# Optimization experiments

Hardware: AMD Instinct MI355X
Metric: run time of the kernel (lower is better)

## Reference

```python
import jax, jax.numpy as jnp
import numpy as np

B, L = 64, 200
NQ = 1024          # n_question == output_dim
NPID = 4096
D = 256            # q_embed_dim
H = 512            # hidden_dim
Q = 1024           # output_dim
L2 = 1e-05


def setup_inputs() -> dict:
    key = jax.random.key(0)
    ks = jax.random.split(key, 20)
    q_data = jax.random.randint(ks[0], (B, L), 1, NQ + 1)          # question ids in [1, NQ]
    ans = jax.random.randint(ks[1], (B, L), 0, 2)
    qa_data = q_data + NQ * ans                                     # encoded (q, answer)
    pid_data = jax.random.randint(ks[2], (B, L), 0, NPID + 1)
    matrix = jax.random.uniform(ks[3], (Q, Q), jnp.float32) * 0.05  # p_c_relations
    u = jax.random.uniform(ks[4], (B, L))
    target = jnp.where(u < 0.1, -1.0, jnp.where(u < 0.55, 0.0, 1.0)).astype(jnp.float32)
    s = 0.05
    q_emb = jax.random.normal(ks[5], (NQ + 1, D), jnp.float32) * s
    qa_emb = jax.random.normal(ks[6], (2, D), jnp.float32) * s
    q_emb_diff = jax.random.normal(ks[7], (NQ + 1, D), jnp.float32) * s
    qa_emb_diff = jax.random.normal(ks[8], (2 * NQ + 1, D), jnp.float32) * s
    diff_parm = jax.random.normal(ks[9], (NPID + 1, 1), jnp.float32) * s
    gs = 1.0 / np.sqrt(H).astype(np.float32)
    w_ih = jax.random.uniform(ks[10], (3 * H, 2 * D), jnp.float32, -gs, gs)
    w_hh = jax.random.uniform(ks[11], (3 * H, H), jnp.float32, -gs, gs)
    b_ih = jax.random.uniform(ks[12], (3 * H,), jnp.float32, -gs, gs)
    b_hh = jax.random.uniform(ks[13], (3 * H,), jnp.float32, -gs, gs)
    fc_w = jax.random.normal(ks[14], (Q, H), jnp.float32) * 0.02
    fc_b = jnp.zeros((Q,), jnp.float32)
    return dict(q_data=q_data, qa_data=qa_data, pid_data=pid_data, matrix=matrix,
                target=target, q_emb=q_emb, qa_emb=qa_emb, q_emb_diff=q_emb_diff,
                qa_emb_diff=qa_emb_diff, diff_parm=diff_parm, w_ih=w_ih, w_hh=w_hh,
                b_ih=b_ih, b_hh=b_hh, fc_w=fc_w, fc_b=fc_b)


def _gru(x, w_ih, w_hh, b_ih, b_hh):
    # PyTorch GRU, single layer, batch_first. x: [B, L, In]
    xg = jnp.einsum('bli,gi->blg', x, w_ih) + b_ih          # [B, L, 3H]
    def step(h, xg_t):
        hg = h @ w_hh.T + b_hh
        xr, xz, xn = jnp.split(xg_t, 3, axis=-1)
        hr, hz, hn = jnp.split(hg, 3, axis=-1)
        r = jax.nn.sigmoid(xr + hr)
        z = jax.nn.sigmoid(xz + hz)
        n = jnp.tanh(xn + r * hn)
        h_new = (1.0 - z) * n + z * h
        return h_new, h_new
    h0 = jnp.zeros((x.shape[0], w_hh.shape[1]), x.dtype)
    _, hs = jax.lax.scan(step, h0, xg.transpose(1, 0, 2))
    return hs.transpose(1, 0, 2)                             # [B, L, H]


def reference(q_data, qa_data, pid_data, matrix, target, q_emb, qa_emb,
              q_emb_diff, qa_emb_diff, diff_parm, w_ih, w_hh, b_ih, b_hh,
              fc_w, fc_b):
    q_embed = q_emb[q_data]                                  # [B, L, D]
    qa = (qa_data - q_data) // NQ                            # answer in {0,1}
    qa_embed = qa_emb[qa] + q_embed
    pid_embed = diff_parm[pid_data]                          # [B, L, 1]
    q_embed2 = q_embed + pid_embed * q_emb_diff[q_data]
    qa_embed2 = qa_embed + pid_embed * qa_emb_diff[qa]
    c_reg = (pid_embed ** 2).sum() * L2

    x = jnp.concatenate([qa_embed2, q_embed2], axis=-1)      # [B, L, 2D]
    gru_out = _gru(x, w_ih, w_hh, b_ih, b_hh)
    gru_out = jnp.einsum('blh,qh->blq', gru_out, fc_w) + fc_b  # [B, L, Q]

    got = jnp.einsum('blq,kq->blk', gru_out, matrix)         # [B, L, Q]
    master = jnp.where(got >= 0.4, 1.0, got)                 # threshold-to-1 only
    # mastery of the question asked at step t: master[b, t, q-1]
    mvals = jnp.take_along_axis(master, (q_data - 1)[..., None], axis=2)[..., 0]  # [B, L]

    f32 = jnp.float32
    eq = (q_data[:, :, None] == q_data[:, None, :]).astype(f32)   # [B, t, k]
    t_idx = jnp.arange(L)
    tri_strict = (t_idx[:, None] > t_idx[None, :]).astype(f32)    # k < t
    tri_incl = (t_idx[:, None] >= t_idx[None, :]).astype(f32)     # k <= t
    mast = (mvals == 1.0).astype(f32)
    notm = (mvals == 0.0).astype(f32)
    qa1 = (qa == 1).astype(f32)
    qa0 = 1.0 - qa1
    base = eq * tri_strict                                        # [B, L, L]
    mc = jnp.einsum('btk,bk->bt', base, qa1 * mast)   # master_correct
    mi = jnp.einsum('btk,bk->bt', base, qa0 * mast)   # master_incorrect
    nmc = jnp.einsum('btk,bk->bt', base, qa0 * notm)  # no_master_correct
    aa = jnp.einsum('btk,tk->bt', eq, tri_incl)       # answered_all (>= 1)

    arB = jnp.arange(B)
    idx = q_data - 1

    def dina_step(carry, xs):
        guess, slip = carry                            # [B, Q] each
        i_t, m_t, qa_t, mc_t, mi_t, nmc_t, aa_t = xs   # [B] each
        g_upd = jnp.where(m_t == 1.0, mc_t / aa_t,
                          jnp.where(qa_t == 0, 1.0 - nmc_t / aa_t, nmc_t / aa_t))
        upd_slip = (m_t == 1.0) & (qa_t == 0)
        new_g = jnp.where(upd_slip, guess[arB, i_t], g_upd)
        new_s = jnp.where(upd_slip, mi_t / aa_t, slip[arB, i_t])
        guess = guess.at[arB, i_t].set(new_g)
        slip = slip.at[arB, i_t].set(new_s)
        p = (1.0 - new_s) * (m_t * new_g + (1.0 - new_s) * (1.0 - m_t))
        return (guess, slip), p

    init = (jnp.zeros((B, Q), f32), jnp.zeros((B, Q), f32))
    xs = (idx.T, mvals.T, qa.T, mc.T, mi.T, nmc.T, aa.T)
    _, ps = jax.lax.scan(dina_step, init, xs)          # [L, B]
    preds = ps.T.reshape(-1)                           # [B*L]

    labels = target.reshape(-1)
    mask = labels > -0.9
    preds_d = jax.lax.stop_gradient(preds)             # torch detaches via torch.tensor()
    mse_sum = (((preds_d - labels) ** 2) * mask.astype(f32)).sum()
    loss = mse_sum + c_reg
    return (loss, jax.nn.sigmoid(preds_d), mask.sum())
```

## Files before the change

### kernel.cpp

```cpp
#include <hip/hip_runtime.h>
#include <hip/hip_bf16.h>
#include <math.h>

#define BB 64
#define LL 200
#define NQ 1024
#define DD 256
#define HH 512
#define QQ 1024
#define G3 1536
#define BL 12800
#define GBLK 256

#define OFF_ACC   ((size_t)0)
#define OFF_CELLS ((size_t)16)
#define OFF_HA    ((size_t)1056)
#define OFF_AQ    (OFF_HA + 65536)
#define OFF_DQ    (OFF_AQ + 1574400)
#define OFF_BQA   (OFF_DQ + 1574400)
#define OFF_CQA   (OFF_BQA + 3072)
#define OFF_WSUM  (OFF_CQA + 3072)
#define OFF_FCWT  (OFF_WSUM + 393216)
#define OFF_M2    (OFF_FCWT + 524288)
#define OFF_MB    (OFF_M2 + 524288)
#define OFF_XG    (OFF_MB + 1024)
#define OFF_GRUT  (OFF_XG + 19660800)
#define OFF_QINT  (OFF_GRUT + 6553600)
#define OFF_QAINT (OFF_QINT + 12800)
#define OFF_PIDF  (OFF_QAINT + 12800)
#define OFF_MVAL  (OFF_PIDF + 12800)
#define OFF_MC    (OFF_MVAL + 12800)
#define OFF_MI    (OFF_MC + 12800)
#define OFF_NMC   (OFF_MI + 12800)
#define OFF_AA    (OFF_NMC + 12800)
#define OFF_PREDS (OFF_AA + 12800)

typedef float f32x4 __attribute__((ext_vector_type(4)));

__device__ __forceinline__ float wave_sum64(float v) {
    #pragma unroll
    for (int o = 32; o > 0; o >>= 1) v += __shfl_down(v, o, 64);
    return v;
}

__device__ __forceinline__ f32x4 llc_load4(const float* p) {
    f32x4 v;
    asm volatile("global_load_dwordx4 %0, %1, off sc0 sc1" : "=v"(v) : "v"(p));
    return v;
}
__device__ __forceinline__ void llc_wait2(f32x4& a, f32x4& b) {
    asm volatile("s_waitcnt vmcnt(0)" : "+v"(a), "+v"(b));
}
__device__ __forceinline__ void llc_store1(float* p, float v) {
    asm volatile("global_store_dword %0, %1, off sc0 sc1" :: "v"(p), "v"(v) : "memory");
}

__device__ __forceinline__ float quad_sum(float v) {
    float t1 = __int_as_float(__builtin_amdgcn_update_dpp(
        0, __float_as_int(v), 0xB1, 0xF, 0xF, true));
    v += t1;
    float t2 = __int_as_float(__builtin_amdgcn_update_dpp(
        0, __float_as_int(v), 0x4E, 0xF, 0xF, true));
    return v + t2;
}

__global__ __launch_bounds__(256) void prep_meta(
    const int* __restrict__ q_data, const int* __restrict__ qa_data,
    const int* __restrict__ pid_data, const float* __restrict__ diff_parm,
    int* __restrict__ qint, int* __restrict__ qaint, float* __restrict__ pidf,
    float* __restrict__ acc)
{
    int r = blockIdx.x * 256 + threadIdx.x;
    float pp = 0.f;
    if (r < BL) {
        int q = q_data[r];
        qint[r] = q;
        qaint[r] = (qa_data[r] - q) / NQ;
        float pid = diff_parm[pid_data[r]];
        pidf[r] = pid;
        pp = pid * pid;
    }
    pp = wave_sum64(pp);
    __shared__ float sm[4];
    int lane = threadIdx.x & 63, w = threadIdx.x >> 6;
    if (lane == 0) sm[w] = pp;
    __syncthreads();
    if (threadIdx.x == 0) atomicAdd(&acc[0], sm[0] + sm[1] + sm[2] + sm[3]);
}

__global__ __launch_bounds__(256) void wsum_kernel(const float* __restrict__ w_ih,
                                                   float* __restrict__ wsum)
{
    int g = blockIdx.x, d = threadIdx.x;
    wsum[(size_t)g * DD + d] = w_ih[(size_t)g * 2 * DD + d] + w_ih[(size_t)g * 2 * DD + DD + d];
}

__global__ __launch_bounds__(256) void transpose_kernel(const float* __restrict__ in,
                                                        float* __restrict__ out, int R, int C)
{
    __shared__ float tile[32][33];
    int r0 = blockIdx.y * 32, c0 = blockIdx.x * 32;
    int tx = threadIdx.x & 31, ty = threadIdx.x >> 5;
    #pragma unroll
    for (int i = 0; i < 32; i += 8) {
        int r = r0 + ty + i, c = c0 + tx;
        if (r < R && c < C) tile[ty + i][tx] = in[(size_t)r * C + c];
    }
    __syncthreads();
    #pragma unroll
    for (int i = 0; i < 32; i += 8) {
        int c = c0 + ty + i, r = r0 + tx;
        if (c < C && r < R) out[(size_t)c * R + r] = tile[tx][ty + i];
    }
}

__global__ __launch_bounds__(256) void gemm_nt_dual(
    const float* __restrict__ A0, const float* __restrict__ A1, int lda,
    const float* __restrict__ B0, const float* __restrict__ B1, int ldb0, int ldb1,
    float* __restrict__ C0, float* __restrict__ C1, int ldc,
    int M, int N, int K,
    const float* __restrict__ bias0, const float* __restrict__ bias1)
{
    const int z = blockIdx.z;
    const float* A = z ? A1 : A0;
    const float* B = z ? B1 : B0;
    float* C = z ? C1 : C0;
    const int ldb = z ? ldb1 : ldb0;
    const float* bias = z ? bias1 : bias0;

    __shared__ float As[16][65];
    __shared__ float Bs[16][65];
    const int bm = blockIdx.y * 64, bn = blockIdx.x * 64;
    const int tid = threadIdx.x;
    const int tx = tid & 15, ty = tid >> 4;
    const int mm = tid >> 4, kk = tid & 15;
    float acc[4][4] = {};
    float ar[4], br[4];
    #pragma unroll
    for (int i = 0; i < 4; ++i) {
        int m = bm + mm + 16 * i;
        ar[i] = (m < M) ? A[(size_t)m * lda + kk] : 0.f;
        int n = bn + mm + 16 * i;
        br[i] = (n < N) ? B[(size_t)n * ldb + kk] : 0.f;
    }
    for (int k0 = 0; k0 < K; k0 += 16) {
        #pragma unroll
        for (int i = 0; i < 4; ++i) { As[kk][mm + 16 * i] = ar[i]; Bs[kk][mm + 16 * i] = br[i]; }
        __syncthreads();
        int kn = k0 + 16;
        if (kn < K) {
            #pragma unroll
            for (int i = 0; i < 4; ++i) {
                int m = bm + mm + 16 * i;
                ar[i] = (m < M) ? A[(size_t)m * lda + kn + kk] : 0.f;
                int n = bn + mm + 16 * i;
                br[i] = (n < N) ? B[(size_t)n * ldb + kn + kk] : 0.f;
            }
        }
        #pragma unroll
        for (int kq = 0; kq < 16; ++kq) {
            float a[4], b[4];
            #pragma unroll
            for (int i = 0; i < 4; ++i) a[i] = As[kq][ty * 4 + i];
            #pragma unroll
            for (int j = 0; j < 4; ++j) b[j] = Bs[kq][tx * 4 + j];
            #pragma unroll
            for (int i = 0; i < 4; ++i)
                #pragma unroll
                for (int j = 0; j < 4; ++j) acc[i][j] += a[i] * b[j];
        }
        __syncthreads();
    }
    #pragma unroll
    for (int i = 0; i < 4; ++i) {
        int m = bm + ty * 4 + i;
        if (m >= M) continue;
        #pragma unroll
        for (int j = 0; j < 4; ++j) {
            int n = bn + tx * 4 + j;
            if (n >= N) continue;
            C[(size_t)m * ldc + n] = acc[i][j] + (bias ? bias[n] : 0.f);
        }
    }
}

__global__ __launch_bounds__(256) void gemm_nt_splitk(
    const float* __restrict__ Ain, int lda,
    const float* __restrict__ Bin, int ldb,
    float* __restrict__ Cp, int ldc,
    int M, int N, int K4)
{
    const int z = blockIdx.z;
    const float* A = Ain + (size_t)z * K4;
    const float* B = Bin + (size_t)z * K4;
    float* C = Cp + (size_t)z * M * ldc;

    __shared__ float As[16][65];
    __shared__ float Bs[16][65];
    const int bm = blockIdx.y * 64, bn = blockIdx.x * 64;
    const int tid = threadIdx.x;
    const int tx = tid & 15, ty = tid >> 4;
    const int mm = tid >> 4, kk = tid & 15;
    float acc[4][4] = {};
    float ar[4], br[4];
    #pragma unroll
    for (int i = 0; i < 4; ++i) {
        int m = bm + mm + 16 * i;
        ar[i] = (m < M) ? A[(size_t)m * lda + kk] : 0.f;
        int n = bn + mm + 16 * i;
        br[i] = (n < N) ? B[(size_t)n * ldb + kk] : 0.f;
    }
    for (int k0 = 0; k0 < K4; k0 += 16) {
        #pragma unroll
        for (int i = 0; i < 4; ++i) { As[kk][mm + 16 * i] = ar[i]; Bs[kk][mm + 16 * i] = br[i]; }
        __syncthreads();
        int kn = k0 + 16;
        if (kn < K4) {
            #pragma unroll
            for (int i = 0; i < 4; ++i) {
                int m = bm + mm + 16 * i;
                ar[i] = (m < M) ? A[(size_t)m * lda + kn + kk] : 0.f;
                int n = bn + mm + 16 * i;
                br[i] = (n < N) ? B[(size_t)n * ldb + kn + kk] : 0.f;
            }
        }
        #pragma unroll
        for (int kq = 0; kq < 16; ++kq) {
            float a[4], b[4];
            #pragma unroll
            for (int i = 0; i < 4; ++i) a[i] = As[kq][ty * 4 + i];
            #pragma unroll
            for (int j = 0; j < 4; ++j) b[j] = Bs[kq][tx * 4 + j];
            #pragma unroll
            for (int i = 0; i < 4; ++i)
                #pragma unroll
                for (int j = 0; j < 4; ++j) acc[i][j] += a[i] * b[j];
        }
        __syncthreads();
    }
    #pragma unroll
    for (int i = 0; i < 4; ++i) {
        int m = bm + ty * 4 + i;
        if (m >= M) continue;
        #pragma unroll
        for (int j = 0; j < 4; ++j) {
            int n = bn + tx * 4 + j;
            if (n >= N) continue;
            C[(size_t)m * ldc + n] = acc[i][j];
        }
    }
}

__global__ __launch_bounds__(256) void reduce4_kernel(const float* __restrict__ p,
                                                      float* __restrict__ o, int n)
{
    int i = blockIdx.x * 256 + threadIdx.x;
    if (i < n) o[i] = p[i] + p[n + i] + p[2 * n + i] + p[3 * n + i];
}

__global__ __launch_bounds__(256) void mb_kernel(const float* __restrict__ matrix,
                                                 const float* __restrict__ fc_b,
                                                 float* __restrict__ mb)
{
    int k = blockIdx.x;
    float s = 0.f;
    for (int q = threadIdx.x; q < QQ; q += 256) s += matrix[(size_t)k * QQ + q] * fc_b[q];
    s = wave_sum64(s);
    __shared__ float sm[4];
    int lane = threadIdx.x & 63, w = threadIdx.x >> 6;
    if (lane == 0) sm[w] = s;
    __syncthreads();
    if (threadIdx.x == 0) mb[k] = sm[0] + sm[1] + sm[2] + sm[3];
}

__global__ __launch_bounds__(512) void xgt_kernel(
    const float* __restrict__ Aq, const float* __restrict__ Bqa,
    const float* __restrict__ Cqa, const float* __restrict__ Dq,
    const int* __restrict__ qint, const int* __restrict__ qaint,
    const float* __restrict__ pidf, float* __restrict__ xgT)
{
    const int t = blockIdx.x;
    __shared__ float tile[64][129];
    __shared__ int qs[BB];
    __shared__ int qas[BB];
    __shared__ float ps[BB];
    const int tid = threadIdx.x;
    if (tid < BB) {
        qs[tid] = qint[tid * LL + t];
        qas[tid] = qaint[tid * LL + t];
        ps[tid] = pidf[tid * LL + t];
    }
    __syncthreads();
    for (int g0 = 0; g0 < G3; g0 += 128) {
        #pragma unroll
        for (int it = 0; it < 16; ++it) {
            int idx = it * 512 + tid;
            int b = idx >> 7, gg = idx & 127;
            int g = g0 + gg;
            int q = qs[b], qa = qas[b];
            float pid = ps[b];
            tile[b][gg] = Aq[(size_t)q * G3 + g] + Bqa[(size_t)qa * G3 + g]
                        + pid * (Cqa[(size_t)qa * G3 + g] + Dq[(size_t)q * G3 + g]);
        }
        __syncthreads();
        #pragma unroll
        for (int it = 0; it < 16; ++it) {
            int idx = it * 512 + tid;
            int gg = idx >> 6, b = idx & 63;
            xgT[((size_t)t * G3 + g0 + gg) * BB + b] = tile[b][gg];
        }
        __syncthreads();
    }
}

__global__ __launch_bounds__(512) void gru_persist(
    const float* __restrict__ xgT,
    const float* __restrict__ w_hh,
    const float* __restrict__ b_hh,
    float* __restrict__ hA,
    float* __restrict__ gruT2,
    unsigned int* __restrict__ cells)
{
    __shared__ float hs[8][512];
    __shared__ float part[8][3][16][8];

    const int tid = threadIdx.x;
    const int bid = blockIdx.x;
    const int bg = bid >> 5;
    const int j0 = (bid & 31) * 16;
    const int wv = tid >> 6;
    const int lane = tid & 63;
    const int g = lane >> 2;
    const int s = lane & 3;

    f32x4 ws4[3][4];
    #pragma unroll
    for (int gate = 0; gate < 3; ++gate) {
        #pragma unroll
        for (int q = 0; q < 4; ++q) {
            ws4[gate][q] = *(const f32x4*)&w_hh[(size_t)(gate * HH + j0 + g) * HH
                                                + wv * 64 + q * 16 + s * 4];
        }
    }

    const int eu = tid >> 3;
    const int eb = tid & 7;
    float bhr = 0.f, bhz = 0.f, bhn = 0.f;
    if (tid < 128) {
        bhr = b_hh[j0 + eu];
        bhz = b_hh[HH + j0 + eu];
        bhn = b_hh[2 * HH + j0 + eu];
    }

    const int b0 = lane >> 4;
    const int c0 = (lane & 15) * 4;

    int cur = 0;
    for (int t = 0; t < LL; ++t) {
        float xr = 0.f, xz = 0.f, xn = 0.f;
        if (tid < 128) {
            const float* xb = xgT + (size_t)t * G3 * BB;
            int col = bg * 8 + eb;
            xr = xb[(size_t)(j0 + eu) * BB + col];
            xz = xb[(size_t)(HH + j0 + eu) * BB + col];
            xn = xb[(size_t)(2 * HH + j0 + eu) * BB + col];
        }
        if (t && tid < 64) {
            const unsigned want = (unsigned)t;
            for (;;) {
                unsigned v = want;
                if (lane < 32)
                    v = __hip_atomic_load(&cells[(bg * 32 + lane) * 4],
                                          __ATOMIC_RELAXED, __HIP_MEMORY_SCOPE_AGENT);
                if (__all((int)(v >= want))) break;
                __builtin_amdgcn_s_sleep(2);
            }
        }
        __syncthreads();

        const float* hcur = hA + (size_t)cur * (HH * BB);
        {
            const float* p0 = hcur + (size_t)(bg * 8 + b0) * HH + wv * 64 + c0;
            f32x4 va = llc_load4(p0);
            f32x4 vb = llc_load4(p0 + 4 * HH);
            llc_wait2(va, vb);
            *(f32x4*)&hs[wv][b0 * 64 + ((c0 + 8 * b0) & 63)] = va;
            *(f32x4*)&hs[wv][(b0 + 4) * 64 + ((c0 + 8 * b0 + 32) & 63)] = vb;
        }

        float acc[3][8];
        #pragma unroll
        for (int gate = 0; gate < 3; ++gate) {
            #pragma unroll
            for (int b = 0; b < 8; ++b) acc[gate][b] = 0.f;
        }
        #pragma unroll
        for (int q = 0; q < 4; ++q) {
            const int cb = q * 16 + s * 4;
            #pragma unroll
            for (int b = 0; b < 8; ++b) {
                f32x4 h4 = *(const f32x4*)&hs[wv][b * 64 + ((cb + 8 * b) & 63)];
                #pragma unroll
                for (int gate = 0; gate < 3; ++gate) {
                    acc[gate][b] += ws4[gate][q].x * h4.x + ws4[gate][q].y * h4.y
                                  + ws4[gate][q].z * h4.z + ws4[gate][q].w * h4.w;
                }
            }
        }

        #pragma unroll
        for (int gate = 0; gate < 3; ++gate) {
            #pragma unroll
            for (int b = 0; b < 8; ++b) acc[gate][b] = quad_sum(acc[gate][b]);
        }

        if (s < 3) {
            const int rot = (2 * ((g >> 2) + s)) & 7;
            #pragma unroll
            for (int hp = 0; hp < 4; ++hp) {
                const int b = hp * 2;
                float e0 = (s == 0) ? acc[0][b]     : (s == 1) ? acc[1][b]     : acc[2][b];
                float e1 = (s == 0) ? acc[0][b + 1] : (s == 1) ? acc[1][b + 1] : acc[2][b + 1];
                const int bp = (b + rot) & 7;
                *(float2*)&part[wv][s][g][bp] = make_float2(e0, e1);
            }
        }
        __syncthreads();

        if (tid < 128) {
            const int rb = eu >> 2;
            const int bp0 = (eb + 2 * (rb + 0)) & 7;
            const int bp1 = (eb + 2 * (rb + 1)) & 7;
            const int bp2 = (eb + 2 * (rb + 2)) & 7;
            float sg0 = 0.f, sg1 = 0.f, sg2 = 0.f;
            #pragma unroll
            for (int w = 0; w < 8; ++w) {
                sg0 += part[w][0][eu][bp0];
                sg1 += part[w][1][eu][bp1];
                sg2 += part[w][2][eu][bp2];
            }
            const int ku = j0 + eu;
            float hprev = hs[ku >> 6][eb * 64 + (((ku & 63) + 8 * eb) & 63)];
            float r = 1.f / (1.f + expf(-(xr + sg0 + bhr)));
            float z = 1.f / (1.f + expf(-(xz + sg1 + bhz)));
            float n = tanhf(xn + r * (sg2 + bhn));
            float hn = (1.f - z) * n + z * hprev;
            llc_store1(hA + (size_t)(cur ^ 1) * (HH * BB) + (size_t)(bg * 8 + eb) * HH + ku, hn);
            gruT2[((size_t)t * BB + bg * 8 + eb) * HH + ku] = hn;
            asm volatile("s_waitcnt vmcnt(0)" ::: "memory");
        }
        __syncthreads();
        if (tid == 0 && t + 1 < LL)
            __hip_atomic_fetch_add(&cells[bid * 4], 1u,
                                   __ATOMIC_RELAXED, __HIP_MEMORY_SCOPE_AGENT);
        cur ^= 1;
    }
}

__global__ __launch_bounds__(256) void mval_kernel(
    const float* __restrict__ gruT2,
    const float* __restrict__ M2,
    const float* __restrict__ mb,
    const int* __restrict__ qint,
    float* __restrict__ mval)
{
    int t = blockIdx.x;
    int wave = threadIdx.x >> 6, l = threadIdx.x & 63;
    for (int ii = 0; ii < 16; ++ii) {
        int b = wave * 16 + ii;
        int q = qint[b * LL + t] - 1;
        const float4* hp = (const float4*)(gruT2 + ((size_t)t * BB + b) * HH);
        const float4* mp = (const float4*)(M2 + (size_t)q * HH);
        float4 h0 = hp[l], m0 = mp[l];
        float4 h1 = hp[64 + l], m1 = mp[64 + l];
        float acc = h0.x * m0.x + h0.y * m0.y + h0.z * m0.z + h0.w * m0.w
                  + h1.x * m1.x + h1.y * m1.y + h1.z * m1.z + h1.w * m1.w;
        acc = wave_sum64(acc);
        if (l == 0) {
            float sv = acc + mb[q];
            mval[b * LL + t] = (sv >= 0.4f) ? 1.0f : sv;
        }
    }
}

__global__ __launch_bounds__(256) void stats_kernel(
    const int* __restrict__ qint, const int* __restrict__ qaint,
    const float* __restrict__ mval,
    float* __restrict__ mc, float* __restrict__ mi,
    float* __restrict__ nmc, float* __restrict__ aa)
{
    int b = blockIdx.x, tid = threadIdx.x;
    __shared__ int qs[LL];
    __shared__ int qas[LL];
    __shared__ float mv[LL];
    if (tid < LL) {
        qs[tid] = qint[b * LL + tid];
        qas[tid] = qaint[b * LL + tid];
        mv[tid] = mval[b * LL + tid];
    }
    __syncthreads();
    int t = tid;
    if (t < LL) {
        int qt = qs[t];
        float smc = 0.f, smi = 0.f, snmc = 0.f, saa = 0.f;
        for (int k = 0; k <= t; ++k) {
            if (qs[k] == qt) {
                saa += 1.f;
                if (k < t) {
                    float mk = (mv[k] == 1.f) ? 1.f : 0.f;
                    float nk = (mv[k] == 0.f) ? 1.f : 0.f;
                    float a1 = (qas[k] == 1) ? 1.f : 0.f;
                    smc += a1 * mk;
                    smi += (1.f - a1) * mk;
                    snmc += (1.f - a1) * nk;
                }
            }
        }
        mc[b * LL + t] = smc;
        mi[b * LL + t] = smi;
        nmc[b * LL + t] = snmc;
        aa[b * LL + t] = saa;
    }
}

__global__ __launch_bounds__(256) void dina_kernel(
    const int* __restrict__ qint, const int* __restrict__ qaint,
    const float* __restrict__ mval,
    const float* __restrict__ mc, const float* __restrict__ mi,
    const float* __restrict__ nmc, const float* __restrict__ aa,
    float* __restrict__ preds)
{
    int b = blockIdx.x, tid = threadIdx.x;
    __shared__ float guess[QQ], slip[QQ];
    __shared__ float s_m[LL], s_mc[LL], s_mi[LL], s_nmc[LL], s_aa[LL];
    __shared__ int s_i[LL], s_qa[LL];
    for (int i = tid; i < QQ; i += 256) { guess[i] = 0.f; slip[i] = 0.f; }
    if (tid < LL) {
        s_m[tid] = mval[b * LL + tid];
        s_mc[tid] = mc[b * LL + tid];
        s_mi[tid] = mi[b * LL + tid];
        s_nmc[tid] = nmc[b * LL + tid];
        s_aa[tid] = aa[b * LL + tid];
        s_i[tid] = qint[b * LL + tid] - 1;
        s_qa[tid] = qaint[b * LL + tid];
    }
    __syncthreads();
    if (tid == 0) {
        for (int t = 0; t < LL; ++t) {
            int i = s_i[t];
            float m = s_m[t];
            int qa = s_qa[t];
            float aat = s_aa[t];
            float g_upd = (m == 1.f) ? s_mc[t] / aat
                          : ((qa == 0) ? 1.f - s_nmc[t] / aat : s_nmc[t] / aat);
            bool us = (m == 1.f) && (qa == 0);
            float ng = us ? guess[i] : g_upd;
            float ns = us ? s_mi[t] / aat : slip[i];
            guess[i] = ng;
            slip[i] = ns;
            preds[b * LL + t] = (1.f - ns) * (m * ng + (1.f - ns) * (1.f - m));
        }
    }
}

__global__ __launch_bounds__(256) void loss_kernel(
    const float* __restrict__ preds, const float* __restrict__ target,
    float* __restrict__ out, float* __restrict__ acc)
{
    int r = blockIdx.x * 256 + threadIdx.x;
    float lm = 0.f, lc = 0.f;
    if (r < BL) {
        float p = preds[r], lab = target[r];
        float msk = (lab > -0.9f) ? 1.f : 0.f;
        float d = p - lab;
        lm = d * d * msk;
        lc = msk;
        out[1 + r] = 1.f / (1.f + expf(-p));
    }
    lm = wave_sum64(lm);
    lc = wave_sum64(lc);
    __shared__ float sm[4], sc[4];
    int lane = threadIdx.x & 63, w = threadIdx.x >> 6;
    if (lane == 0) { sm[w] = lm; sc[w] = lc; }
    __syncthreads();
    if (threadIdx.x == 0) {
        atomicAdd(&acc[1], sm[0] + sm[1] + sm[2] + sm[3]);
        atomicAdd(&acc[2], sc[0] + sc[1] + sc[2] + sc[3]);
    }
}

__global__ void final_kernel(const float* __restrict__ acc, float* __restrict__ out)
{
    out[0] = acc[1] + acc[0] * 1e-5f;
    out[1 + BL] = acc[2];
}

extern "C" void kernel_launch(void* const* d_in, const int* in_sizes, int n_in,
                              void* d_out, int out_size, void* d_ws, size_t ws_size,
                              hipStream_t stream) {
    const int* q_data = (const int*)d_in[0];
    const int* qa_data = (const int*)d_in[1];
    const int* pid_data = (const int*)d_in[2];
    const float* matrix = (const float*)d_in[3];
    const float* target = (const float*)d_in[4];
    const float* q_emb = (const float*)d_in[5];
    const float* qa_emb = (const float*)d_in[6];
    const float* q_emb_diff = (const float*)d_in[7];
    const float* qa_emb_diff = (const float*)d_in[8];
    const float* diff_parm = (const float*)d_in[9];
    const float* w_ih = (const float*)d_in[10];
    const float* w_hh = (const float*)d_in[11];
    const float* b_ih = (const float*)d_in[12];
    const float* b_hh = (const float*)d_in[13];
    const float* fc_w = (const float*)d_in[14];
    const float* fc_b = (const float*)d_in[15];
    float* out = (float*)d_out;
    float* W = (float*)d_ws;

    float* acc = W + OFF_ACC;
    unsigned int* cells = (unsigned int*)(W + OFF_CELLS);
    float* hA = W + OFF_HA;
    float* Aq = W + OFF_AQ;
    float* Dq = W + OFF_DQ;
    float* Bqa = W + OFF_BQA;
    float* Cqa = W + OFF_CQA;
    float* wsum = W + OFF_WSUM;
    float* fcwT = W + OFF_FCWT;
    float* M2 = W + OFF_M2;
    float* mb = W + OFF_MB;
    float* xgT = W + OFF_XG;
    float* m2parts = W + OFF_XG;
    float* gruT2 = W + OFF_GRUT;
    int* qint = (int*)(W + OFF_QINT);
    int* qaint = (int*)(W + OFF_QAINT);
    float* pidf = W + OFF_PIDF;
    float* mval = W + OFF_MVAL;
    float* mc = W + OFF_MC;
    float* mi = W + OFF_MI;
    float* nmc = W + OFF_NMC;
    float* aa = W + OFF_AA;
    float* preds = W + OFF_PREDS;

    hipMemsetAsync(W, 0, (OFF_HA + 2 * HH * BB) * sizeof(float), stream);

    prep_meta<<<50, 256, 0, stream>>>(q_data, qa_data, pid_data, diff_parm,
                                      qint, qaint, pidf, acc);
    wsum_kernel<<<G3, 256, 0, stream>>>(w_ih, wsum);
    transpose_kernel<<<dim3(16, 32), 256, 0, stream>>>(fc_w, fcwT, QQ, HH);

    gemm_nt_dual<<<dim3(24, 1, 2), 256, 0, stream>>>(
        qa_emb, qa_emb_diff, DD, w_ih, w_ih, 2 * DD, 2 * DD,
        Bqa, Cqa, G3, 2, G3, DD, b_ih, nullptr);
    gemm_nt_dual<<<dim3(24, 17, 2), 256, 0, stream>>>(
        q_emb, q_emb_diff, DD, wsum, w_ih + DD, DD, 2 * DD,
        Aq, Dq, G3, NQ + 1, G3, DD, nullptr, nullptr);
    gemm_nt_splitk<<<dim3(8, 16, 4), 256, 0, stream>>>(
        matrix, QQ, fcwT, QQ, m2parts, HH, QQ, HH, QQ / 4);
    reduce4_kernel<<<2048, 256, 0, stream>>>(m2parts, M2, QQ * HH);
    mb_kernel<<<QQ, 256, 0, stream>>>(matrix, fc_b, mb);

    xgt_kernel<<<LL, 512, 0, stream>>>(Aq, Bqa, Cqa, Dq, qint, qaint, pidf, xgT);

    gru_persist<<<GBLK, 512, 0, stream>>>(xgT, w_hh, b_hh, hA, gruT2, cells);

    mval_kernel<<<LL, 256, 0, stream>>>(gruT2, M2, mb, qint, mval);
    stats_kernel<<<BB, 256, 0, stream>>>(qint, qaint, mval, mc, mi, nmc, aa);
    dina_kernel<<<BB, 256, 0, stream>>>(qint, qaint, mval, mc, mi, nmc, aa, preds);
    loss_kernel<<<50, 256, 0, stream>>>(preds, target, out, acc);
    final_kernel<<<1, 1, 0, stream>>>(acc, out);
}
```

Baseline: 1.160 ms.

## Compute M2 and mb in extra blocks of the persistent GRU kernel

Removes the separate transpose, split-K GEMM, reduce and mb kernels. Their work (matrix·fc_wᵀ and matrix·fc_b) now runs in 130 extra worker blocks appended to the persistent GRU launch, so it overlaps with the latency-bound recurrence. GRU blocks raise their wave priority with s_setprio. The step counter now uses an atomic store of t+1 instead of an atomic add. The risk is that worker blocks take CU resources or memory bandwidth from GRU blocks. If the 386 blocks are not all resident at once, the spin-wait sync could also be affected.

```diff
diff --git a/kernel.cpp b/kernel.cpp
--- a/kernel.cpp
+++ b/kernel.cpp
@@ -11,6 +11,7 @@
 #define G3 1536
 #define BL 12800
 #define GBLK 256
+#define NWRK 130
 
 #define OFF_ACC   ((size_t)0)
 #define OFF_CELLS ((size_t)16)
@@ -95,25 +96,6 @@
     wsum[(size_t)g * DD + d] = w_ih[(size_t)g * 2 * DD + d] + w_ih[(size_t)g * 2 * DD + DD + d];
 }
 
-__global__ __launch_bounds__(256) void transpose_kernel(const float* __restrict__ in,
-                                                        float* __restrict__ out, int R, int C)
-{
-    __shared__ float tile[32][33];
-    int r0 = blockIdx.y * 32, c0 = blockIdx.x * 32;
-    int tx = threadIdx.x & 31, ty = threadIdx.x >> 5;
-    #pragma unroll
-    for (int i = 0; i < 32; i += 8) {
-        int r = r0 + ty + i, c = c0 + tx;
-        if (r < R && c < C) tile[ty + i][tx] = in[(size_t)r * C + c];
-    }
-    __syncthreads();
-    #pragma unroll
-    for (int i = 0; i < 32; i += 8) {
-        int c = c0 + ty + i, r = r0 + tx;
-        if (c < C && r < R) out[(size_t)c * R + r] = tile[tx][ty + i];
-    }
-}
-
 __global__ __launch_bounds__(256) void gemm_nt_dual(
     const float* __restrict__ A0, const float* __restrict__ A1, int lda,
     const float* __restrict__ B0, const float* __restrict__ B1, int ldb0, int ldb1,
@@ -184,95 +166,6 @@
     }
 }
 
-__global__ __launch_bounds__(256) void gemm_nt_splitk(
-    const float* __restrict__ Ain, int lda,
-    const float* __restrict__ Bin, int ldb,
-    float* __restrict__ Cp, int ldc,
-    int M, int N, int K4)
-{
-    const int z = blockIdx.z;
-    const float* A = Ain + (size_t)z * K4;
-    const float* B = Bin + (size_t)z * K4;
-    float* C = Cp + (size_t)z * M * ldc;
-
-    __shared__ float As[16][65];
-    __shared__ float Bs[16][65];
-    const int bm = blockIdx.y * 64, bn = blockIdx.x * 64;
-    const int tid = threadIdx.x;
-    const int tx = tid & 15, ty = tid >> 4;
-    const int mm = tid >> 4, kk = tid & 15;
-    float acc[4][4] = {};
-    float ar[4], br[4];
-    #pragma unroll
-    for (int i = 0; i < 4; ++i) {
-        int m = bm + mm + 16 * i;
-        ar[i] = (m < M) ? A[(size_t)m * lda + kk] : 0.f;
-        int n = bn + mm + 16 * i;
-        br[i] = (n < N) ? B[(size_t)n * ldb + kk] : 0.f;
-    }
-    for (int k0 = 0; k0 < K4; k0 += 16) {
-        #pragma unroll
-        for (int i = 0; i < 4; ++i) { As[kk][mm + 16 * i] = ar[i]; Bs[kk][mm + 16 * i] = br[i]; }
-        __syncthreads();
-        int kn = k0 + 16;
-        if (kn < K4) {
-            #pragma unroll
-            for (int i = 0; i < 4; ++i) {
-                int m = bm + mm + 16 * i;
-                ar[i] = (m < M) ? A[(size_t)m * lda + kn + kk] : 0.f;
-                int n = bn + mm + 16 * i;
-                br[i] = (n < N) ? B[(size_t)n * ldb + kn + kk] : 0.f;
-            }
-        }
-        #pragma unroll
-        for (int kq = 0; kq < 16; ++kq) {
-            float a[4], b[4];
-            #pragma unroll
-            for (int i = 0; i < 4; ++i) a[i] = As[kq][ty * 4 + i];
-            #pragma unroll
-            for (int j = 0; j < 4; ++j) b[j] = Bs[kq][tx * 4 + j];
-            #pragma unroll
-            for (int i = 0; i < 4; ++i)
-                #pragma unroll
-                for (int j = 0; j < 4; ++j) acc[i][j] += a[i] * b[j];
-        }
-        __syncthreads();
-    }
-    #pragma unroll
-    for (int i = 0; i < 4; ++i) {
-        int m = bm + ty * 4 + i;
-        if (m >= M) continue;
-        #pragma unroll
-        for (int j = 0; j < 4; ++j) {
-            int n = bn + tx * 4 + j;
-            if (n >= N) continue;
-            C[(size_t)m * ldc + n] = acc[i][j];
-        }
-    }
-}
-
-__global__ __launch_bounds__(256) void reduce4_kernel(const float* __restrict__ p,
-                                                      float* __restrict__ o, int n)
-{
-    int i = blockIdx.x * 256 + threadIdx.x;
-    if (i < n) o[i] = p[i] + p[n + i] + p[2 * n + i] + p[3 * n + i];
-}
-
-__global__ __launch_bounds__(256) void mb_kernel(const float* __restrict__ matrix,
-                                                 const float* __restrict__ fc_b,
-                                                 float* __restrict__ mb)
-{
-    int k = blockIdx.x;
-    float s = 0.f;
-    for (int q = threadIdx.x; q < QQ; q += 256) s += matrix[(size_t)k * QQ + q] * fc_b[q];
-    s = wave_sum64(s);
-    __shared__ float sm[4];
-    int lane = threadIdx.x & 63, w = threadIdx.x >> 6;
-    if (lane == 0) sm[w] = s;
-    __syncthreads();
-    if (threadIdx.x == 0) mb[k] = sm[0] + sm[1] + sm[2] + sm[3];
-}
-
 __global__ __launch_bounds__(512) void xgt_kernel(
     const float* __restrict__ Aq, const float* __restrict__ Bqa,
     const float* __restrict__ Cqa, const float* __restrict__ Dq,
@@ -319,13 +212,70 @@
     const float* __restrict__ b_hh,
     float* __restrict__ hA,
     float* __restrict__ gruT2,
-    unsigned int* __restrict__ cells)
+    unsigned int* __restrict__ cells,
+    const float* __restrict__ matrix,
+    const float* __restrict__ fc_w,
+    const float* __restrict__ fc_b,
+    float* __restrict__ M2,
+    float* __restrict__ mb)
 {
     __shared__ float hs[8][512];
     __shared__ float part[8][3][16][8];
+    __shared__ float As[16][65];
+    __shared__ float Bs[16][65];
 
     const int tid = threadIdx.x;
     const int bid = blockIdx.x;
+
+    if (bid >= GBLK) {
+        const int widx = bid - GBLK;
+        if (widx >= 128) {
+            const int wv2 = tid >> 6, lane2 = tid & 63;
+            const int kb = (widx - 128) * 512 + wv2 * 64;
+            for (int i = 0; i < 64; ++i) {
+                const float* mrow = matrix + (size_t)(kb + i) * QQ;
+                float sacc = 0.f;
+                #pragma unroll
+                for (int j = 0; j < 16; ++j)
+                    sacc += mrow[lane2 + 64 * j] * fc_b[lane2 + 64 * j];
+                sacc = wave_sum64(sacc);
+                if (lane2 == 0) mb[kb + i] = sacc;
+            }
+            return;
+        }
+        const int bm = (widx >> 3) * 64, bn = (widx & 7) * 64;
+        const int mm = tid >> 4, kk = tid & 15;
+        const int nn = tid & 31, k2 = tid >> 5;
+        const int tx = tid & 15, ty = tid >> 4;
+        float acc[2][4] = {};
+        for (int k0 = 0; k0 < QQ; k0 += 16) {
+            if (k0) __syncthreads();
+            As[kk][mm]      = matrix[(size_t)(bm + mm) * QQ + k0 + kk];
+            As[kk][mm + 32] = matrix[(size_t)(bm + mm + 32) * QQ + k0 + kk];
+            Bs[k2][nn]      = fc_w[(size_t)(k0 + k2) * HH + bn + nn];
+            Bs[k2][nn + 32] = fc_w[(size_t)(k0 + k2) * HH + bn + nn + 32];
+            __syncthreads();
+            #pragma unroll
+            for (int kq = 0; kq < 16; ++kq) {
+                float a0 = As[kq][ty * 2], a1 = As[kq][ty * 2 + 1];
+                #pragma unroll
+                for (int j = 0; j < 4; ++j) {
+                    float bv = Bs[kq][tx * 4 + j];
+                    acc[0][j] += a0 * bv;
+                    acc[1][j] += a1 * bv;
+                }
+            }
+        }
+        #pragma unroll
+        for (int i = 0; i < 2; ++i)
+            #pragma unroll
+            for (int j = 0; j < 4; ++j)
+                M2[(size_t)(bm + ty * 2 + i) * HH + bn + tx * 4 + j] = acc[i][j];
+        return;
+    }
+
+    __builtin_amdgcn_s_setprio(1);
+
     const int bg = bid >> 5;
     const int j0 = (bid & 31) * 16;
     const int wv = tid >> 6;
@@ -335,13 +285,11 @@
 
     f32x4 ws4[3][4];
     #pragma unroll
-    for (int gate = 0; gate < 3; ++gate) {
-        #pragma unroll
-        for (int q = 0; q < 4; ++q) {
-            ws4[gate][q] = *(const f32x4*)&w_hh[(size_t)(gate * HH + j0 + g) * HH
-                                                + wv * 64 + q * 16 + s * 4];
-        }
-    }
+    for (int gate = 0; gate < 3; ++gate)
+        #pragma unroll
+        for (int q = 0; q < 4; ++q)
+            ws4[gate][q] = *(const f32x4*)&w_hh[
+                (size_t)(gate * HH + j0 + g) * HH + wv * 64 + q * 16 + s * 4];
 
     const int eu = tid >> 3;
     const int eb = tid & 7;
@@ -355,7 +303,6 @@
     const int b0 = lane >> 4;
     const int c0 = (lane & 15) * 4;
 
-    int cur = 0;
     for (int t = 0; t < LL; ++t) {
         float xr = 0.f, xz = 0.f, xn = 0.f;
         if (tid < 128) {
@@ -378,8 +325,8 @@
         }
         __syncthreads();
 
-        const float* hcur = hA + (size_t)cur * (HH * BB);
         {
+            const float* hcur = hA + (size_t)(t & 1) * (HH * BB);
             const float* p0 = hcur + (size_t)(bg * 8 + b0) * HH + wv * 64 + c0;
             f32x4 va = llc_load4(p0);
             f32x4 vb = llc_load4(p0 + 4 * HH);
@@ -409,10 +356,10 @@
         }
 
         #pragma unroll
-        for (int gate = 0; gate < 3; ++gate) {
-            #pragma unroll
-            for (int b = 0; b < 8; ++b) acc[gate][b] = quad_sum(acc[gate][b]);
-        }
+        for (int gate = 0; gate < 3; ++gate)
+            #pragma unroll
+            for (int b = 0; b < 8; ++b)
+                acc[gate][b] = quad_sum(acc[gate][b]);
 
         if (s < 3) {
             const int rot = (2 * ((g >> 2) + s)) & 7;
@@ -441,19 +388,19 @@
             }
             const int ku = j0 + eu;
             float hprev = hs[ku >> 6][eb * 64 + (((ku & 63) + 8 * eb) & 63)];
-            float r = 1.f / (1.f + expf(-(xr + sg0 + bhr)));
-            float z = 1.f / (1.f + expf(-(xz + sg1 + bhz)));
-            float n = tanhf(xn + r * (sg2 + bhn));
-            float hn = (1.f - z) * n + z * hprev;
-            llc_store1(hA + (size_t)(cur ^ 1) * (HH * BB) + (size_t)(bg * 8 + eb) * HH + ku, hn);
+            float rg = 1.f / (1.f + expf(-(xr + sg0 + bhr)));
+            float zg = 1.f / (1.f + expf(-(xz + sg1 + bhz)));
+            float ng = tanhf(xn + rg * (sg2 + bhn));
+            float hn = (1.f - zg) * ng + zg * hprev;
+            llc_store1(hA + (size_t)((t + 1) & 1) * (HH * BB)
+                          + (size_t)(bg * 8 + eb) * HH + ku, hn);
             gruT2[((size_t)t * BB + bg * 8 + eb) * HH + ku] = hn;
             asm volatile("s_waitcnt vmcnt(0)" ::: "memory");
         }
         __syncthreads();
         if (tid == 0 && t + 1 < LL)
-            __hip_atomic_fetch_add(&cells[bid * 4], 1u,
-                                   __ATOMIC_RELAXED, __HIP_MEMORY_SCOPE_AGENT);
-        cur ^= 1;
+            __hip_atomic_store(&cells[bid * 4], (unsigned)(t + 1),
+                               __ATOMIC_RELAXED, __HIP_MEMORY_SCOPE_AGENT);
     }
 }
 
@@ -625,11 +572,9 @@
     float* Bqa = W + OFF_BQA;
     float* Cqa = W + OFF_CQA;
     float* wsum = W + OFF_WSUM;
-    float* fcwT = W + OFF_FCWT;
     float* M2 = W + OFF_M2;
     float* mb = W + OFF_MB;
     float* xgT = W + OFF_XG;
-    float* m2parts = W + OFF_XG;
     float* gruT2 = W + OFF_GRUT;
     int* qint = (int*)(W + OFF_QINT);
     int* qaint = (int*)(W + OFF_QAINT);
@@ -646,7 +591,6 @@
     prep_meta<<<50, 256, 0, stream>>>(q_data, qa_data, pid_data, diff_parm,
                                       qint, qaint, pidf, acc);
     wsum_kernel<<<G3, 256, 0, stream>>>(w_ih, wsum);
-    transpose_kernel<<<dim3(16, 32), 256, 0, stream>>>(fc_w, fcwT, QQ, HH);
 
     gemm_nt_dual<<<dim3(24, 1, 2), 256, 0, stream>>>(
         qa_emb, qa_emb_diff, DD, w_ih, w_ih, 2 * DD, 2 * DD,
@@ -654,14 +598,11 @@
     gemm_nt_dual<<<dim3(24, 17, 2), 256, 0, stream>>>(
         q_emb, q_emb_diff, DD, wsum, w_ih + DD, DD, 2 * DD,
         Aq, Dq, G3, NQ + 1, G3, DD, nullptr, nullptr);
-    gemm_nt_splitk<<<dim3(8, 16, 4), 256, 0, stream>>>(
-        matrix, QQ, fcwT, QQ, m2parts, HH, QQ, HH, QQ / 4);
-    reduce4_kernel<<<2048, 256, 0, stream>>>(m2parts, M2, QQ * HH);
-    mb_kernel<<<QQ, 256, 0, stream>>>(matrix, fc_b, mb);
 
     xgt_kernel<<<LL, 512, 0, stream>>>(Aq, Bqa, Cqa, Dq, qint, qaint, pidf, xgT);
 
-    gru_persist<<<GBLK, 512, 0, stream>>>(xgT, w_hh, b_hh, hA, gruT2, cells);
+    gru_persist<<<GBLK + NWRK, 512, 0, stream>>>(xgT, w_hh, b_hh, hA, gruT2, cells,
+                                                 matrix, fc_w, fc_b, M2, mb);
 
     mval_kernel<<<LL, 256, 0, stream>>>(gruT2, M2, mb, qint, mval);
     stats_kernel<<<BB, 256, 0, stream>>>(qint, qaint, mval, mc, mi, nmc, aa);
```

After: 1.184 ms. +2.1%, slower.
